# Optimization experiments

Measured on AMD Instinct MI355X. Metric: run time of the kernel, lower is better.

Reference implementation:

```python
import jax, jax.numpy as jnp
import numpy as np

N_NODES = 100000
N_EDGES = 6400000
NUM_FEATURES = 128
NUM_CLASSES = 4


def _gcn_conv(x, W, b, src, dst, n):
    # PyG GCNConv: h = x @ W, symmetric norm over edges (self-loops already added),
    # scatter-add messages to dst, then add bias.
    h = x @ W                                            # [N, out]
    deg = jax.ops.segment_sum(jnp.ones(dst.shape[0], x.dtype), dst, num_segments=n)
    dinv = jnp.where(deg > 0, jax.lax.rsqrt(deg), 0.0)   # deg^-1/2, 0 for isolated
    norm = dinv[src] * dinv[dst]                         # [E]
    agg = jax.ops.segment_sum(h[src] * norm[:, None], dst, num_segments=n)
    return agg + b


def setup_inputs() -> dict:
    key = jax.random.key(0)
    ks = jax.random.split(key, 10)
    x = jax.random.normal(ks[0], (N_NODES, NUM_FEATURES), dtype=jnp.float32)
    edge_index = jax.random.randint(ks[1], (2, N_EDGES), 0, N_NODES, dtype=jnp.int32)

    def lin(k, fan_in, fan_out):
        s = 1.0 / np.sqrt(fan_in)
        return jax.random.uniform(k, (fan_in, fan_out), jnp.float32, -s, s)

    return {
        "x": x,
        "edge_index": edge_index,
        "W1": lin(ks[2], NUM_FEATURES, 4), "b1": jnp.zeros((4,), jnp.float32),
        "W2": lin(ks[3], 4, 4),            "b2": jnp.zeros((4,), jnp.float32),
        "W3": lin(ks[4], 4, 2),            "b3": jnp.zeros((2,), jnp.float32),
        "Wc": lin(ks[5], 2, NUM_CLASSES),  "bc": jnp.zeros((NUM_CLASSES,), jnp.float32),
    }


def reference(x, edge_index, W1, b1, W2, b2, W3, b3, Wc, bc):
    n = x.shape[0]
    loops = jnp.arange(n, dtype=edge_index.dtype)
    src = jnp.concatenate([edge_index[0], loops])  # add self-loops once; graph fixed across layers
    dst = jnp.concatenate([edge_index[1], loops])

    h = jnp.tanh(_gcn_conv(x, W1, b1, src, dst, n))
    h = jnp.tanh(_gcn_conv(h, W2, b2, src, dst, n))
    h = jnp.tanh(_gcn_conv(h, W3, b3, src, dst, n))
    out = h @ Wc + bc
    return (out, h)
```

## Files before the change

### kernel.cpp

```cpp
#include <hip/hip_runtime.h>
#include <math.h>


#define LCHUNK 16384
#define CHUNK2 16000
#define MAXNB  512
#define CAP    18432
#define MAXNB2 1024
#define CAP2   9600

__device__ __forceinline__ int swz_chunk(int bid, int G) {
    if ((G & 7) != 0) return bid;
    return (bid & 7) * (G >> 3) + (bid >> 3);
}

__global__ __launch_bounds__(1024) void k_local(
        const int* __restrict__ src, const int* __restrict__ dst,
        int* __restrict__ packed, int* __restrict__ hbT, int* __restrict__ loff,
        int NBK, int G, int e) {
    __shared__ int hist[MAXNB];
    __shared__ int cur[MAXNB];
    __shared__ int part[1024];
    __shared__ int stage[LCHUNK];
    int g = blockIdx.x, tid = threadIdx.x;
    for (int b = tid; b < NBK; b += 1024) hist[b] = 0;
    __syncthreads();
    int i0 = g * LCHUNK;
    int i1 = min(i0 + LCHUNK, e);
    int val[16], bkt[16];
#pragma unroll
    for (int k = 0; k < 16; k++) {
        int i = i0 + tid + (k << 10);
        bool v = i < i1;
        int d = v ? dst[i] : 0;
        int s = v ? src[i] : 0;
        bkt[k] = v ? (d >> 8) : -1;
        val[k] = ((d & 255) << 17) | s;
        if (v) atomicAdd(&hist[d >> 8], 1);
    }
    __syncthreads();
    int s0 = (tid < NBK) ? hist[tid] : 0;
    part[tid] = s0;
    __syncthreads();
#pragma unroll
    for (int off = 1; off < 1024; off <<= 1) {
        int u = (tid >= off) ? part[tid - off] : 0;
        __syncthreads();
        part[tid] += u;
        __syncthreads();
    }
    int excl = part[tid] - s0;
    if (tid < NBK) {
        cur[tid] = excl;
        hbT[(size_t)tid * G + g] = s0;
        loff[(size_t)g * NBK + tid] = excl;
    }
    __syncthreads();
#pragma unroll
    for (int k = 0; k < 16; k++) {
        if (bkt[k] >= 0) {
            int p = atomicAdd(&cur[bkt[k]], 1);
            stage[p] = val[k];
        }
    }
    __syncthreads();
    int len = i1 - i0;
    for (int i = tid; i < len; i += 1024)
        packed[i0 + i] = stage[i];
}

__global__ void k_scanA(int* __restrict__ hbT, int* __restrict__ btot, int G) {
    __shared__ int part[256];
    int b = blockIdx.x, t = threadIdx.x;
    int* row = hbT + (size_t)b * G;
    int C = (G + 255) / 256;
    int lo = t * C, hi = min(lo + C, G);
    int s = 0;
    for (int i = lo; i < hi; i++) s += row[i];
    part[t] = s;
    __syncthreads();
#pragma unroll
    for (int off = 1; off < 256; off <<= 1) {
        int u = (t >= off) ? part[t - off] : 0;
        __syncthreads();
        part[t] += u;
        __syncthreads();
    }
    int run = part[t] - s;
    for (int i = lo; i < hi; i++) {
        int v = row[i];
        row[i] = run;
        run += v;
    }
    if (t == 255) btot[b] = part[255];
}

__global__ void k_scanB(const int* __restrict__ btot, int* __restrict__ bstart,
                        int NB, int e) {
    __shared__ int part[512];
    int t = threadIdx.x;
    int C = (NB + 511) / 512;
    int lo = t * C, hi = min(lo + C, NB);
    int s = 0;
    for (int i = lo; i < hi; i++) s += btot[i];
    part[t] = s;
    __syncthreads();
#pragma unroll
    for (int off = 1; off < 512; off <<= 1) {
        int u = (t >= off) ? part[t - off] : 0;
        __syncthreads();
        part[t] += u;
        __syncthreads();
    }
    int run = part[t] - s;
    for (int i = lo; i < hi; i++) {
        bstart[i] = run;
        run += btot[i];
    }
    if (t == 511) bstart[NB] = e;
}

__global__ __launch_bounds__(512) void k_merge(
        const int* __restrict__ hbT, const int* __restrict__ loff,
        const int* __restrict__ btot, const int* __restrict__ bstart,
        const int* __restrict__ packed, int* __restrict__ csr,
        float* __restrict__ dinv, int* __restrict__ rowoff,
        int NBK, int G, int n) {
    __shared__ int stage[CAP];
    __shared__ int stage2[CAP];
    __shared__ int cnt[256];
    __shared__ int off[256];
    __shared__ int cur[256];
    int b = blockIdx.x, tid = threadIdx.x;
    int btt = btot[b];
    int total = min(btt, CAP);
    for (int g = tid; g < G; g += 512) {
        int o  = hbT[(size_t)b * G + g];
        int nx = (g + 1 < G) ? hbT[(size_t)b * G + g + 1] : btt;
        if (nx > CAP) nx = CAP;
        if (o >= nx) continue;
        int len = nx - o;
        int sp = g * LCHUNK + loff[(size_t)g * NBK + b];
        int a   = sp & ~3;
        int rel = sp - a;
        int n4  = (rel + len + 3) >> 2;
        for (int q = 0; q < n4; q++) {
            int4 w = *reinterpret_cast<const int4*>(packed + a + q * 4);
            int base = q * 4 - rel;
            if (base >= 0 && base < len)     stage[o + base]     = w.x;
            if (base + 1 >= 0 && base + 1 < len) stage[o + base + 1] = w.y;
            if (base + 2 >= 0 && base + 2 < len) stage[o + base + 2] = w.z;
            if (base + 3 >= 0 && base + 3 < len) stage[o + base + 3] = w.w;
        }
    }
    if (tid < 256) cnt[tid] = 0;
    __syncthreads();
    for (int i = tid; i < total; i += 512) atomicAdd(&cnt[stage[i] >> 17], 1);
    __syncthreads();
    if (tid < 256) off[tid] = cnt[tid];
    __syncthreads();
#pragma unroll
    for (int s = 1; s < 256; s <<= 1) {
        int v = 0;
        if (tid < 256 && tid >= s) v = off[tid - s];
        __syncthreads();
        if (tid < 256 && tid >= s) off[tid] += v;
        __syncthreads();
    }
    if (tid < 256) {
        int excl = off[tid] - cnt[tid];
        int node = (b << 8) + tid;
        if (node < n) dinv[node] = 1.0f / sqrtf((float)(cnt[tid] + 1));
        if (node <= n) rowoff[node] = bstart[b] + excl;
        cur[tid] = excl;
    }
    __syncthreads();
    for (int i = tid; i < total; i += 512) {
        int w = stage[i];
        int p = atomicAdd(&cur[w >> 17], 1);
        stage2[p] = w & 0x1FFFF;
    }
    __syncthreads();
    int base = bstart[b];
    for (int i = tid; i < total; i += 512)
        csr[base + i] = stage2[i];
}

__global__ void k_hist_o(const int* __restrict__ dst, int* __restrict__ hbT,
                         int NB, int G, int e) {
    __shared__ int hist[MAXNB2];
    int g = swz_chunk(blockIdx.x, G);
    for (int b = threadIdx.x; b < NB; b += 512) hist[b] = 0;
    __syncthreads();
    long long i0 = (long long)g * CHUNK2;
    int i1 = (int)min(i0 + CHUNK2, (long long)e);
    for (int i = (int)i0 + threadIdx.x; i < i1; i += 512)
        atomicAdd(&hist[dst[i] >> 7], 1);
    __syncthreads();
    for (int b = threadIdx.x; b < NB; b += 512)
        hbT[(size_t)b * G + g] = hist[b];
}

__global__ void k_part_o(const int* __restrict__ src, const int* __restrict__ dst,
                         const int* __restrict__ hbT, const int* __restrict__ bstart,
                         int* __restrict__ packed, int NB, int G, int e) {
    __shared__ int cur[MAXNB2];
    int g = swz_chunk(blockIdx.x, G);
    for (int b = threadIdx.x; b < NB; b += 512)
        cur[b] = hbT[(size_t)b * G + g] + bstart[b];
    __syncthreads();
    long long i0 = (long long)g * CHUNK2;
    int i1 = (int)min(i0 + CHUNK2, (long long)e);
    for (int i = (int)i0 + threadIdx.x; i < i1; i += 512) {
        int d = dst[i], s = src[i];
        int pos = atomicAdd(&cur[d >> 7], 1);
        packed[pos] = ((d & 127) << 17) | s;
    }
}

__global__ void k_build_o(const int* __restrict__ bstart, int* __restrict__ packed,
                          float* __restrict__ dinv, int* __restrict__ rowoff, int n) {
    __shared__ int stage[CAP2];
    __shared__ int cnt[128];
    __shared__ int off[128];
    __shared__ int cur[128];
    int b = blockIdx.x, tid = threadIdx.x;
    int lo = bstart[b];
    int len = bstart[b + 1] - lo;
    if (len > CAP2) len = CAP2;
    if (tid < 128) cnt[tid] = 0;
    for (int i = tid; i < len; i += 256) stage[i] = packed[lo + i];
    __syncthreads();
    for (int i = tid; i < len; i += 256) atomicAdd(&cnt[stage[i] >> 17], 1);
    __syncthreads();
    if (tid < 128) off[tid] = cnt[tid];
    __syncthreads();
#pragma unroll
    for (int s = 1; s < 128; s <<= 1) {
        int v = 0;
        if (tid < 128 && tid >= s) v = off[tid - s];
        __syncthreads();
        if (tid < 128 && tid >= s) off[tid] += v;
        __syncthreads();
    }
    if (tid < 128) {
        int excl = off[tid] - cnt[tid];
        int node = (b << 7) + tid;
        if (node < n) dinv[node] = 1.0f / sqrtf((float)(cnt[tid] + 1));
        if (node <= n) rowoff[node] = lo + excl;
        cur[tid] = excl;
    }
    __syncthreads();
    for (int i = tid; i < len; i += 256) {
        int w = stage[i];
        int p = atomicAdd(&cur[w >> 17], 1);
        packed[lo + p] = w & 0x1FFFF;
    }
}

__global__ void k_mm1(const float* __restrict__ x, const float* __restrict__ W,
                      const float* __restrict__ dinv, float* __restrict__ hs, int n) {
    int gid = blockIdx.x * blockDim.x + threadIdx.x;
    int node = gid >> 6;
    int lane = threadIdx.x & 63;
    if (node >= n) return;
    const float2 xv = *reinterpret_cast<const float2*>(x + (size_t)node * 128 + lane * 2);
    const float4 w0 = *reinterpret_cast<const float4*>(W + (lane * 2) * 4);
    const float4 w1 = *reinterpret_cast<const float4*>(W + (lane * 2 + 1) * 4);
    float a0 = xv.x * w0.x + xv.y * w1.x;
    float a1 = xv.x * w0.y + xv.y * w1.y;
    float a2 = xv.x * w0.z + xv.y * w1.z;
    float a3 = xv.x * w0.w + xv.y * w1.w;
#pragma unroll
    for (int m = 32; m >= 1; m >>= 1) {
        a0 += __shfl_xor(a0, m);
        a1 += __shfl_xor(a1, m);
        a2 += __shfl_xor(a2, m);
        a3 += __shfl_xor(a3, m);
    }
    if (lane == 0) {
        float di = dinv[node];
        *reinterpret_cast<float4*>(hs + (size_t)node * 4) =
            make_float4(a0 * di, a1 * di, a2 * di, a3 * di);
    }
}

__global__ void k_gath4(const int* __restrict__ rowoff, const int* __restrict__ csr,
                        const float* __restrict__ hs, float* __restrict__ agg, int n) {
    int gid = blockIdx.x * blockDim.x + threadIdx.x;
    int node = gid >> 4;
    int sub = threadIdx.x & 15;
    if (node >= n) return;
    int start = rowoff[node], end = rowoff[node + 1];
    float a0 = 0.f, a1 = 0.f, a2 = 0.f, a3 = 0.f;
    for (int j = start + sub; j < end; j += 16) {
        int s = csr[j];
        float4 v = *reinterpret_cast<const float4*>(hs + (size_t)s * 4);
        a0 += v.x; a1 += v.y; a2 += v.z; a3 += v.w;
    }
#pragma unroll
    for (int m = 8; m >= 1; m >>= 1) {
        a0 += __shfl_xor(a0, m);
        a1 += __shfl_xor(a1, m);
        a2 += __shfl_xor(a2, m);
        a3 += __shfl_xor(a3, m);
    }
    if (sub == 0)
        *reinterpret_cast<float4*>(agg + (size_t)node * 4) =
            make_float4(a0, a1, a2, a3);
}

__global__ void k_gath2(const int* __restrict__ rowoff, const int* __restrict__ csr,
                        const float* __restrict__ hs, float* __restrict__ agg, int n) {
    int gid = blockIdx.x * blockDim.x + threadIdx.x;
    int node = gid >> 4;
    int sub = threadIdx.x & 15;
    if (node >= n) return;
    int start = rowoff[node], end = rowoff[node + 1];
    float a0 = 0.f, a1 = 0.f;
    for (int j = start + sub; j < end; j += 16) {
        int s = csr[j];
        float2 v = *reinterpret_cast<const float2*>(hs + (size_t)s * 2);
        a0 += v.x; a1 += v.y;
    }
#pragma unroll
    for (int m = 8; m >= 1; m >>= 1) {
        a0 += __shfl_xor(a0, m);
        a1 += __shfl_xor(a1, m);
    }
    if (sub == 0)
        *reinterpret_cast<float2*>(agg + (size_t)node * 2) = make_float2(a0, a1);
}

template <int FOUT>
__global__ void k_fin4(const float* __restrict__ agg, const float* __restrict__ hs,
                       const float* __restrict__ dinv, const float* __restrict__ b_,
                       const float* __restrict__ Wn, float* __restrict__ hsn, int n) {
    int i = blockIdx.x * blockDim.x + threadIdx.x;
    if (i >= n) return;
    float4 a = *reinterpret_cast<const float4*>(agg + (size_t)i * 4);
    float4 s = *reinterpret_cast<const float4*>(hs + (size_t)i * 4);
    float di = dinv[i];
    float h0 = tanhf((a.x + s.x) * di + b_[0]);
    float h1 = tanhf((a.y + s.y) * di + b_[1]);
    float h2 = tanhf((a.z + s.z) * di + b_[2]);
    float h3 = tanhf((a.w + s.w) * di + b_[3]);
    float o[FOUT];
#pragma unroll
    for (int j = 0; j < FOUT; j++) {
        o[j] = (h0 * Wn[0 * FOUT + j] + h1 * Wn[1 * FOUT + j] +
                h2 * Wn[2 * FOUT + j] + h3 * Wn[3 * FOUT + j]) * di;
    }
    if constexpr (FOUT == 4) {
        *reinterpret_cast<float4*>(hsn + (size_t)i * 4) =
            make_float4(o[0], o[1], o[2], o[3]);
    } else {
        *reinterpret_cast<float2*>(hsn + (size_t)i * 2) = make_float2(o[0], o[1]);
    }
}

__global__ void k_fin3(const float* __restrict__ agg, const float* __restrict__ hs,
                       const float* __restrict__ dinv, const float* __restrict__ b3,
                       const float* __restrict__ Wc, const float* __restrict__ bc,
                       float* __restrict__ out, float* __restrict__ hout, int n) {
    int i = blockIdx.x * blockDim.x + threadIdx.x;
    if (i >= n) return;
    float2 a = *reinterpret_cast<const float2*>(agg + (size_t)i * 2);
    float2 s = *reinterpret_cast<const float2*>(hs + (size_t)i * 2);
    float di = dinv[i];
    float h0 = tanhf((a.x + s.x) * di + b3[0]);
    float h1 = tanhf((a.y + s.y) * di + b3[1]);
    *reinterpret_cast<float2*>(hout + (size_t)i * 2) = make_float2(h0, h1);
    float4 o;
    o.x = h0 * Wc[0] + h1 * Wc[4] + bc[0];
    o.y = h0 * Wc[1] + h1 * Wc[5] + bc[1];
    o.z = h0 * Wc[2] + h1 * Wc[6] + bc[2];
    o.w = h0 * Wc[3] + h1 * Wc[7] + bc[3];
    *reinterpret_cast<float4*>(out + (size_t)i * 4) = o;
}

extern "C" void kernel_launch(void* const* d_in, const int* in_sizes, int n_in,
                              void* d_out, int out_size, void* d_ws, size_t ws_size,
                              hipStream_t stream) {
    const float* x  = (const float*)d_in[0];
    const int*  ei  = (const int*)d_in[1];
    const float* W1 = (const float*)d_in[2];
    const float* b1 = (const float*)d_in[3];
    const float* W2 = (const float*)d_in[4];
    const float* b2 = (const float*)d_in[5];
    const float* W3 = (const float*)d_in[6];
    const float* b3 = (const float*)d_in[7];
    const float* Wc = (const float*)d_in[8];
    const float* bc = (const float*)d_in[9];

    const int n = in_sizes[0] / 128;
    const int e = in_sizes[1] / 2;
    const int* src = ei;
    const int* dst = ei + e;

    const size_t MB = 1024 * 1024;
    char* ws = (char*)d_ws;
    float* dinv   = (float*)(ws + 0);
    float* hsA    = (float*)(ws + MB / 2);
    float* hsB    = (float*)(ws + 2 * MB + MB / 2);
    int*   rowoff = (int*)  (ws + 4 * MB + MB / 2);
    int*   btot   = (int*)  (ws + 5 * MB);
    int*   bstart = (int*)  (ws + 5 * MB + 16 * 1024);
    int*   hbT    = (int*)  (ws + 5 * MB + MB / 2);
    float* agg    = (float*)(ws + 8 * MB);
    int*   loff   = (int*)  (ws + 10 * MB);
    int*   packed = (int*)  (ws + 12 * MB);
    int*   csr    = (int*)  (ws + 38 * MB);

    float* out  = (float*)d_out;
    float* hout = out + (size_t)n * 4;

    const size_t need_new = 38 * MB + (size_t)e * 4 + MB;
    const bool use_new = ws_size >= need_new;

    const int* csr_p;
    if (use_new) {
        const int NBK = (n + 255) >> 8;
        const int G = (e + LCHUNK - 1) / LCHUNK;
        k_local<<<G, 1024, 0, stream>>>(src, dst, packed, hbT, loff, NBK, G, e);
        k_scanA<<<NBK, 256, 0, stream>>>(hbT, btot, G);
        k_scanB<<<1, 512, 0, stream>>>(btot, bstart, NBK, e);
        k_merge<<<NBK, 512, 0, stream>>>(hbT, loff, btot, bstart, packed, csr,
                                         dinv, rowoff, NBK, G, n);
        csr_p = csr;
    } else {
        const int NB2 = (n + 127) >> 7;
        const int G2 = (e + CHUNK2 - 1) / CHUNK2;
        k_hist_o<<<G2, 512, 0, stream>>>(dst, hbT, NB2, G2, e);
        k_scanA<<<NB2, 256, 0, stream>>>(hbT, btot, G2);
        k_scanB<<<1, 512, 0, stream>>>(btot, bstart, NB2, e);
        k_part_o<<<G2, 512, 0, stream>>>(src, dst, hbT, bstart, packed, NB2, G2, e);
        k_build_o<<<NB2, 256, 0, stream>>>(bstart, packed, dinv, rowoff, n);
        csr_p = packed;
    }

    const int wb = (n + 3) / 4;
    const int qb = (n + 15) / 16;
    const int nb = (n + 255) / 256;
    k_mm1<<<wb, 256, 0, stream>>>(x, W1, dinv, hsA, n);

    k_gath4<<<qb, 256, 0, stream>>>(rowoff, csr_p, hsA, agg, n);
    k_fin4<4><<<nb, 256, 0, stream>>>(agg, hsA, dinv, b1, W2, hsB, n);
    k_gath4<<<qb, 256, 0, stream>>>(rowoff, csr_p, hsB, agg, n);
    k_fin4<2><<<nb, 256, 0, stream>>>(agg, hsB, dinv, b2, W3, hsA, n);
    k_gath2<<<qb, 256, 0, stream>>>(rowoff, csr_p, hsA, agg, n);
    k_fin3<<<nb, 256, 0, stream>>>(agg, hsA, dinv, b3, Wc, bc, out, hout, n);

    (void)n_in; (void)out_size;
}
```

Baseline: 201.4 us.

## Split CSR build into histogram pass plus direct global scatter by bucket

```diff
diff --git a/kernel.cpp b/kernel.cpp
--- a/kernel.cpp
+++ b/kernel.cpp
@@ -14,59 +14,19 @@
     return (bid & 7) * (G >> 3) + (bid >> 3);
 }
 
-__global__ __launch_bounds__(1024) void k_local(
-        const int* __restrict__ src, const int* __restrict__ dst,
-        int* __restrict__ packed, int* __restrict__ hbT, int* __restrict__ loff,
-        int NBK, int G, int e) {
+__global__ __launch_bounds__(512) void k_hist(
+        const int* __restrict__ dst, int* __restrict__ hbT, int NBK, int G, int e) {
     __shared__ int hist[MAXNB];
-    __shared__ int cur[MAXNB];
-    __shared__ int part[1024];
-    __shared__ int stage[LCHUNK];
     int g = blockIdx.x, tid = threadIdx.x;
-    for (int b = tid; b < NBK; b += 1024) hist[b] = 0;
+    for (int b = tid; b < NBK; b += 512) hist[b] = 0;
     __syncthreads();
     int i0 = g * LCHUNK;
     int i1 = min(i0 + LCHUNK, e);
-    int val[16], bkt[16];
-#pragma unroll
-    for (int k = 0; k < 16; k++) {
-        int i = i0 + tid + (k << 10);
-        bool v = i < i1;
-        int d = v ? dst[i] : 0;
-        int s = v ? src[i] : 0;
-        bkt[k] = v ? (d >> 8) : -1;
-        val[k] = ((d & 255) << 17) | s;
-        if (v) atomicAdd(&hist[d >> 8], 1);
-    }
-    __syncthreads();
-    int s0 = (tid < NBK) ? hist[tid] : 0;
-    part[tid] = s0;
-    __syncthreads();
-#pragma unroll
-    for (int off = 1; off < 1024; off <<= 1) {
-        int u = (tid >= off) ? part[tid - off] : 0;
-        __syncthreads();
-        part[tid] += u;
-        __syncthreads();
-    }
-    int excl = part[tid] - s0;
-    if (tid < NBK) {
-        cur[tid] = excl;
-        hbT[(size_t)tid * G + g] = s0;
-        loff[(size_t)g * NBK + tid] = excl;
-    }
-    __syncthreads();
-#pragma unroll
-    for (int k = 0; k < 16; k++) {
-        if (bkt[k] >= 0) {
-            int p = atomicAdd(&cur[bkt[k]], 1);
-            stage[p] = val[k];
-        }
-    }
-    __syncthreads();
-    int len = i1 - i0;
-    for (int i = tid; i < len; i += 1024)
-        packed[i0 + i] = stage[i];
+    for (int i = i0 + tid; i < i1; i += 512)
+        atomicAdd(&hist[dst[i] >> 8], 1);
+    __syncthreads();
+    for (int b = tid; b < NBK; b += 512)
+        hbT[(size_t)b * G + g] = hist[b];
 }
 
 __global__ void k_scanA(int* __restrict__ hbT, int* __restrict__ btot, int G) {
@@ -120,42 +80,136 @@
     if (t == 511) bstart[NB] = e;
 }
 
-__global__ __launch_bounds__(512) void k_merge(
-        const int* __restrict__ hbT, const int* __restrict__ loff,
+__global__ __launch_bounds__(1024) void k_place(
+        const int* __restrict__ src, const int* __restrict__ dst,
+        const int* __restrict__ hbT, const int* __restrict__ bstart,
+        int* __restrict__ ctmp, int NBK, int G, int e) {
+    __shared__ int hist[MAXNB];
+    __shared__ int cur[MAXNB];
+    __shared__ int gbase[MAXNB];
+    __shared__ int part[1024];
+    __shared__ int stage[LCHUNK];
+    int g = blockIdx.x, tid = threadIdx.x;
+    for (int b = tid; b < NBK; b += 1024) hist[b] = 0;
+    __syncthreads();
+    int i0 = g * LCHUNK;
+    int i1 = min(i0 + LCHUNK, e);
+    int val[16], bkt[16];
+#pragma unroll
+    for (int k = 0; k < 16; k++) {
+        int i = i0 + tid + (k << 10);
+        bool v = i < i1;
+        int d = v ? dst[i] : 0;
+        int s = v ? src[i] : 0;
+        bkt[k] = v ? (d >> 8) : -1;
+        val[k] = ((d & 255) << 17) | s;
+        if (v) atomicAdd(&hist[d >> 8], 1);
+    }
+    __syncthreads();
+    int s0 = (tid < NBK) ? hist[tid] : 0;
+    part[tid] = s0;
+    __syncthreads();
+#pragma unroll
+    for (int off = 1; off < 1024; off <<= 1) {
+        int u = (tid >= off) ? part[tid - off] : 0;
+        __syncthreads();
+        part[tid] += u;
+        __syncthreads();
+    }
+    int excl = part[tid] - s0;
+    if (tid < NBK) {
+        cur[tid] = excl;
+        gbase[tid] = bstart[tid] + hbT[(size_t)tid * G + g] - excl;
+    }
+    __syncthreads();
+#pragma unroll
+    for (int k = 0; k < 16; k++) {
+        if (bkt[k] >= 0) {
+            int p = atomicAdd(&cur[bkt[k]], 1);
+            stage[p] = val[k];
+        }
+    }
+    __syncthreads();
+    int len = i1 - i0;
+    for (int i = tid; i < len; i += 1024) {
+        int w = stage[i];
+        ctmp[gbase[w >> 17 >> 0 ? (w >> 17) >= 0 ? 0 : 0 : 0] + 0] = 0;
+    }
+    (void)ctmp;
+}
+
+__global__ __launch_bounds__(1024) void k_place2(
+        const int* __restrict__ src, const int* __restrict__ dst,
+        const int* __restrict__ hbT, const int* __restrict__ bstart,
+        int* __restrict__ ctmp, int NBK, int G, int e) {
+    __shared__ int hist[MAXNB];
+    __shared__ int cur[MAXNB];
+    __shared__ int gbase[MAXNB];
+    __shared__ int part[1024];
+    __shared__ int stage[LCHUNK];
+    __shared__ unsigned short sbkt[LCHUNK];
+    int g = blockIdx.x, tid = threadIdx.x;
+    for (int b = tid; b < NBK; b += 1024) hist[b] = 0;
+    __syncthreads();
+    int i0 = g * LCHUNK;
+    int i1 = min(i0 + LCHUNK, e);
+    int val[16], bkt[16];
+#pragma unroll
+    for (int k = 0; k < 16; k++) {
+        int i = i0 + tid + (k << 10);
+        bool v = i < i1;
+        int d = v ? dst[i] : 0;
+        int s = v ? src[i] : 0;
+        bkt[k] = v ? (d >> 8) : -1;
+        val[k] = ((d & 255) << 17) | s;
+        if (v) atomicAdd(&hist[d >> 8], 1);
+    }
+    __syncthreads();
+    int s0 = (tid < NBK) ? hist[tid] : 0;
+    part[tid] = s0;
+    __syncthreads();
+#pragma unroll
+    for (int off = 1; off < 1024; off <<= 1) {
+        int u = (tid >= off) ? part[tid - off] : 0;
+        __syncthreads();
+        part[tid] += u;
+        __syncthreads();
+    }
+    int excl = part[tid] - s0;
+    if (tid < NBK) {
+        cur[tid] = excl;
+        gbase[tid] = bstart[tid] + hbT[(size_t)tid * G + g] - excl;
+    }
+    __syncthreads();
+#pragma unroll
+    for (int k = 0; k < 16; k++) {
+        if (bkt[k] >= 0) {
+            int p = atomicAdd(&cur[bkt[k]], 1);
+            stage[p] = val[k];
+            sbkt[p] = (unsigned short)bkt[k];
+        }
+    }
+    __syncthreads();
+    int len = i1 - i0;
+    for (int i = tid; i < len; i += 1024)
+        ctmp[gbase[sbkt[i]] + i] = stage[i];
+}
+
+__global__ __launch_bounds__(512) void k_nodesort(
         const int* __restrict__ btot, const int* __restrict__ bstart,
-        const int* __restrict__ packed, int* __restrict__ csr,
-        float* __restrict__ dinv, int* __restrict__ rowoff,
-        int NBK, int G, int n) {
-    __shared__ int stage[CAP];
+        const int* __restrict__ ctmp, int* __restrict__ csr,
+        float* __restrict__ dinv, int* __restrict__ rowoff, int n) {
     __shared__ int stage2[CAP];
     __shared__ int cnt[256];
     __shared__ int off[256];
     __shared__ int cur[256];
     int b = blockIdx.x, tid = threadIdx.x;
-    int btt = btot[b];
-    int total = min(btt, CAP);
-    for (int g = tid; g < G; g += 512) {
-        int o  = hbT[(size_t)b * G + g];
-        int nx = (g + 1 < G) ? hbT[(size_t)b * G + g + 1] : btt;
-        if (nx > CAP) nx = CAP;
-        if (o >= nx) continue;
-        int len = nx - o;
-        int sp = g * LCHUNK + loff[(size_t)g * NBK + b];
-        int a   = sp & ~3;
-        int rel = sp - a;
-        int n4  = (rel + len + 3) >> 2;
-        for (int q = 0; q < n4; q++) {
-            int4 w = *reinterpret_cast<const int4*>(packed + a + q * 4);
-            int base = q * 4 - rel;
-            if (base >= 0 && base < len)     stage[o + base]     = w.x;
-            if (base + 1 >= 0 && base + 1 < len) stage[o + base + 1] = w.y;
-            if (base + 2 >= 0 && base + 2 < len) stage[o + base + 2] = w.z;
-            if (base + 3 >= 0 && base + 3 < len) stage[o + base + 3] = w.w;
-        }
-    }
+    int total = min(btot[b], CAP);
+    int base = bstart[b];
     if (tid < 256) cnt[tid] = 0;
     __syncthreads();
-    for (int i = tid; i < total; i += 512) atomicAdd(&cnt[stage[i] >> 17], 1);
+    for (int i = tid; i < total; i += 512)
+        atomicAdd(&cnt[ctmp[base + i] >> 17], 1);
     __syncthreads();
     if (tid < 256) off[tid] = cnt[tid];
     __syncthreads();
@@ -171,17 +225,16 @@
         int excl = off[tid] - cnt[tid];
         int node = (b << 8) + tid;
         if (node < n) dinv[node] = 1.0f / sqrtf((float)(cnt[tid] + 1));
-        if (node <= n) rowoff[node] = bstart[b] + excl;
+        if (node <= n) rowoff[node] = base + excl;
         cur[tid] = excl;
     }
     __syncthreads();
     for (int i = tid; i < total; i += 512) {
-        int w = stage[i];
+        int w = ctmp[base + i];
         int p = atomicAdd(&cur[w >> 17], 1);
         stage2[p] = w & 0x1FFFF;
     }
     __syncthreads();
-    int base = bstart[b];
     for (int i = tid; i < total; i += 512)
         csr[base + i] = stage2[i];
 }
@@ -408,8 +461,7 @@
     int*   bstart = (int*)  (ws + 5 * MB + 16 * 1024);
     int*   hbT    = (int*)  (ws + 5 * MB + MB / 2);
     float* agg    = (float*)(ws + 8 * MB);
-    int*   loff   = (int*)  (ws + 10 * MB);
-    int*   packed = (int*)  (ws + 12 * MB);
+    int*   ctmp   = (int*)  (ws + 12 * MB);
     int*   csr    = (int*)  (ws + 38 * MB);
 
     float* out  = (float*)d_out;
@@ -422,11 +474,12 @@
     if (use_new) {
         const int NBK = (n + 255) >> 8;
         const int G = (e + LCHUNK - 1) / LCHUNK;
-        k_local<<<G, 1024, 0, stream>>>(src, dst, packed, hbT, loff, NBK, G, e);
+        k_hist<<<G, 512, 0, stream>>>(dst, hbT, NBK, G, e);
         k_scanA<<<NBK, 256, 0, stream>>>(hbT, btot, G);
         k_scanB<<<1, 512, 0, stream>>>(btot, bstart, NBK, e);
-        k_merge<<<NBK, 512, 0, stream>>>(hbT, loff, btot, bstart, packed, csr,
-                                         dinv, rowoff, NBK, G, n);
+        k_place2<<<G, 1024, 0, stream>>>(src, dst, hbT, bstart, ctmp, NBK, G, e);
+        k_nodesort<<<NBK, 512, 0, stream>>>(btot, bstart, ctmp, csr,
+                                            dinv, rowoff, n);
         csr_p = csr;
     } else {
         const int NB2 = (n + 127) >> 7;
@@ -434,9 +487,9 @@
         k_hist_o<<<G2, 512, 0, stream>>>(dst, hbT, NB2, G2, e);
         k_scanA<<<NB2, 256, 0, stream>>>(hbT, btot, G2);
         k_scanB<<<1, 512, 0, stream>>>(btot, bstart, NB2, e);
-        k_part_o<<<G2, 512, 0, stream>>>(src, dst, hbT, bstart, packed, NB2, G2, e);
-        k_build_o<<<NB2, 256, 0, stream>>>(bstart, packed, dinv, rowoff, n);
-        csr_p = packed;
+        k_part_o<<<G2, 512, 0, stream>>>(src, dst, hbT, bstart, ctmp, NB2, G2, e);
+        k_build_o<<<NB2, 256, 0, stream>>>(bstart, ctmp, dinv, rowoff, n);
+        csr_p = ctmp;
     }
 
     const int wb = (n + 3) / 4;
```

Result: slower. 215.7 us (+7.1%).
